# Kernel optimization log

Hardware: AMD Instinct MI355X
Metric: run time of the kernel (lower is better)

## Reference

```python
import jax, jax.numpy as jnp
import numpy as np

N, K, F_IN, F_OUT, P = 50000, 32, 64, 64, 3


def setup_inputs() -> dict:
    key = jax.random.key(0)
    k1, k2, k3, k4, k5 = jax.random.split(key, 5)
    h = jax.random.normal(k1, (N, F_IN), dtype=jnp.float32)
    pos = jax.random.normal(k2, (N, P), dtype=jnp.float32)
    neighbor_idx = jax.random.randint(k3, (N, K), 0, N, dtype=jnp.int32)
    weight = jax.random.normal(k4, (K * F_IN, F_OUT), dtype=jnp.float32) * 0.02
    bias_p = jax.random.normal(k5, (1, F_OUT), dtype=jnp.float32) * 0.02
    return {"h": h, "pos": pos, "neighbor_idx": neighbor_idx,
            "weight": weight, "bias_p": bias_p}


def reference(h, pos, neighbor_idx, weight, bias_p):
    n, k = neighbor_idx.shape
    msgs = h[neighbor_idx]                      # [N, K, F_IN] gather
    diff = pos[:, None, :] - pos[neighbor_idx]  # [N, K, P]
    sq = jnp.sum(diff * diff, axis=2, keepdims=True)  # [N, K, 1]
    # torch: dist[dist==0] = 0.5 ; safe-sqrt avoids NaN grads at 0
    dist = jnp.where(sq == 0.0, 0.5, jnp.sqrt(jnp.where(sq == 0.0, 1.0, sq)))
    wow = (msgs / dist).reshape(n, k * h.shape[1])  # [N, K*F_IN]
    h1 = wow @ weight + bias_p                   # [N, F_OUT]
    return jax.nn.leaky_relu(h1, negative_slope=0.01)
```

## Files before the change

### kernel.cpp

```cpp
#include <hip/hip_runtime.h>


#define N_NODES 50000
#define KN      32
#define FIN     64
#define FOUT    64
#define MTILE   64

typedef __attribute__((ext_vector_type(4))) float    f32x4;
typedef __attribute__((ext_vector_type(8))) _Float16 f16x8;

static __device__ __forceinline__ f16x8 dec8i(unsigned int x, unsigned int y) {
    union { unsigned int w[4]; f16x8 v; } r;
    unsigned int xh = x >> 16, yh = y >> 16;
    r.w[0] = 0x64006400u | ((x  & 0xFFu) << 2) | ((x  & 0xFF00u) << 10);
    r.w[1] = 0x64006400u | ((xh & 0xFFu) << 2) | ((xh & 0xFF00u) << 10);
    r.w[2] = 0x64006400u | ((y  & 0xFFu) << 2) | ((y  & 0xFF00u) << 10);
    r.w[3] = 0x64006400u | ((yh & 0xFFu) << 2) | ((yh & 0xFF00u) << 10);
    return r.v;
}

__global__ void k_prep(const float* __restrict__ w, _Float16* __restrict__ wf,
                       const float* __restrict__ h, unsigned char* __restrict__ hq,
                       const float* __restrict__ pos, float4* __restrict__ posx) {
    __shared__ float s_w[64 * 64];
    const int tid = threadIdx.x;
    if (blockIdx.x < 32) {
        const int kn = blockIdx.x;
        for (int p = tid; p < 64 * 64; p += 256)
            s_w[p] = w[kn * 64 * 64 + p];
        __syncthreads();
        const int t = tid >> 6, lane = tid & 63;
        const int lm = lane & 15, q = lane >> 4;
        #pragma unroll
        for (int jh = 0; jh < 2; ++jh) {
            f16x8 o;
            #pragma unroll
            for (int i = 0; i < 8; ++i)
                o[i] = (_Float16)s_w[(q * 16 + jh * 8 + i) * 64 + t * 16 + lm];
            *(f16x8*)(wf + ((kn * 2 + jh) * 4 + t) * 512 + lane * 8) = o;
        }
    } else {
        const int r   = (blockIdx.x - 32) * 64 + (tid >> 2);
        const int sub = tid & 3;
        if (r < N_NODES) {
            const float* hr = h + (size_t)r * FIN + sub * 16;
            float v[16];
            float amax = 0.f;
            #pragma unroll
            for (int i = 0; i < 4; ++i) {
                float4 t4 = ((const float4*)hr)[i];
                v[i * 4 + 0] = t4.x; v[i * 4 + 1] = t4.y;
                v[i * 4 + 2] = t4.z; v[i * 4 + 3] = t4.w;
                amax = fmaxf(amax, fmaxf(fmaxf(fabsf(t4.x), fabsf(t4.y)),
                                         fmaxf(fabsf(t4.z), fabsf(t4.w))));
            }
            amax = fmaxf(amax, __shfl_xor(amax, 1));
            amax = fmaxf(amax, __shfl_xor(amax, 2));
            float scale = fmaxf(amax, 1e-30f) * (1.0f / 126.0f);
            float inv   = 126.0f / fmaxf(amax, 1e-30f);
            union { unsigned char c[16]; uint4 u4; } o;
            #pragma unroll
            for (int i = 0; i < 16; ++i) {
                int q8 = __float2int_rn(v[i] * inv);
                o.c[i] = (unsigned char)(q8 + 128);
            }
            *(uint4*)(hq + (size_t)r * 64 + sub * 16) = o.u4;
            if (sub == 0) {
                float4 px;
                px.x = pos[r * 3 + 0]; px.y = pos[r * 3 + 1]; px.z = pos[r * 3 + 2];
                px.w = scale;
                posx[r] = px;
            }
        }
    }
}

__global__ __launch_bounds__(256, 3) void k_main(
        const unsigned char* __restrict__ hq,
        const float4*        __restrict__ posx,
        const int*           __restrict__ nidx,
        const _Float16*      __restrict__ wf,
        const float*         __restrict__ bias,
        float*               __restrict__ out)
{
    __shared__ __align__(16) char smem[2 * 64 * 68 * 4];
    int2*  s_e   = (int2*)smem;
    float* s_red = (float*)smem;

    const int tid = threadIdx.x;
    const int m0  = blockIdx.x * MTILE;

    for (int p = tid; p < MTILE * KN; p += 256) {
        int m = p & 63, k = p >> 6;
        int node = m0 + m;
        int idx = 0; float c1 = 0.f;
        if (node < N_NODES) {
            idx = nidx[node * KN + k];
            float4 pn = posx[node];
            float4 pi = posx[idx];
            float dx = pn.x - pi.x, dy = pn.y - pi.y, dz = pn.z - pi.z;
            float sq = dx * dx + dy * dy + dz * dz;
            float scl = (sq == 0.f) ? 2.0f : rsqrtf(sq);
            c1 = pi.w * scl * 0.25f;
        }
        s_e[k * MTILE + m] = make_int2(idx, __float_as_int(c1));
    }
    __syncthreads();

    const int lane = tid & 63, kg = tid >> 6;
    const int lm = lane & 15, q = lane >> 4;

    const _Float16* pb = wf + lane * 8;

    f32x4 acc[4][4] = {};

    const int kn0 = kg * 8;
    int2 e0 = s_e[kn0 * MTILE + lm];
    int2 e1 = s_e[kn0 * MTILE + 16 + lm];
    int2 e2 = s_e[kn0 * MTILE + 32 + lm];
    int2 e3 = s_e[kn0 * MTILE + 48 + lm];
    uint4 d0 = *(const uint4*)(hq + (size_t)e0.x * 64 + q * 16);
    uint4 d1 = *(const uint4*)(hq + (size_t)e1.x * 64 + q * 16);
    uint4 d2 = *(const uint4*)(hq + (size_t)e2.x * 64 + q * 16);
    uint4 d3 = *(const uint4*)(hq + (size_t)e3.x * 64 + q * 16);

    #pragma unroll 1
    for (int j = 0; j < 8; ++j) {
        const int kn = kg * 8 + j;

        int2 ne0, ne1, ne2, ne3;
        uint4 nd0, nd1, nd2, nd3;
        if (j < 7) {
            const int knn = kn + 1;
            ne0 = s_e[knn * MTILE + lm];
            ne1 = s_e[knn * MTILE + 16 + lm];
            ne2 = s_e[knn * MTILE + 32 + lm];
            ne3 = s_e[knn * MTILE + 48 + lm];
            nd0 = *(const uint4*)(hq + (size_t)ne0.x * 64 + q * 16);
            nd1 = *(const uint4*)(hq + (size_t)ne1.x * 64 + q * 16);
            nd2 = *(const uint4*)(hq + (size_t)ne2.x * 64 + q * 16);
            nd3 = *(const uint4*)(hq + (size_t)ne3.x * 64 + q * 16);
        }

        const _Float16 c0 = (_Float16)__int_as_float(e0.y);
        const _Float16 c1 = (_Float16)__int_as_float(e1.y);
        const _Float16 c2 = (_Float16)__int_as_float(e2.y);
        const _Float16 c3 = (_Float16)__int_as_float(e3.y);
        const _Float16 K = (_Float16)1536.0f;

        {
            const _Float16* pbb = pb + (kn * 2 + 0) * 2048;
            f16x8 b0 = *(const f16x8*)(pbb);
            f16x8 b1 = *(const f16x8*)(pbb + 512);
            f16x8 b2 = *(const f16x8*)(pbb + 1024);
            f16x8 b3 = *(const f16x8*)(pbb + 1536);
            f16x8 a0 = (dec8i(d0.x, d0.y) - K) * c0;
            f16x8 a1 = (dec8i(d1.x, d1.y) - K) * c1;
            f16x8 a2 = (dec8i(d2.x, d2.y) - K) * c2;
            f16x8 a3 = (dec8i(d3.x, d3.y) - K) * c3;
            acc[0][0] = __builtin_amdgcn_mfma_f32_16x16x32_f16(a0, b0, acc[0][0], 0, 0, 0);
            acc[0][1] = __builtin_amdgcn_mfma_f32_16x16x32_f16(a0, b1, acc[0][1], 0, 0, 0);
            acc[0][2] = __builtin_amdgcn_mfma_f32_16x16x32_f16(a0, b2, acc[0][2], 0, 0, 0);
            acc[0][3] = __builtin_amdgcn_mfma_f32_16x16x32_f16(a0, b3, acc[0][3], 0, 0, 0);
            acc[1][0] = __builtin_amdgcn_mfma_f32_16x16x32_f16(a1, b0, acc[1][0], 0, 0, 0);
            acc[1][1] = __builtin_amdgcn_mfma_f32_16x16x32_f16(a1, b1, acc[1][1], 0, 0, 0);
            acc[1][2] = __builtin_amdgcn_mfma_f32_16x16x32_f16(a1, b2, acc[1][2], 0, 0, 0);
            acc[1][3] = __builtin_amdgcn_mfma_f32_16x16x32_f16(a1, b3, acc[1][3], 0, 0, 0);
            acc[2][0] = __builtin_amdgcn_mfma_f32_16x16x32_f16(a2, b0, acc[2][0], 0, 0, 0);
            acc[2][1] = __builtin_amdgcn_mfma_f32_16x16x32_f16(a2, b1, acc[2][1], 0, 0, 0);
            acc[2][2] = __builtin_amdgcn_mfma_f32_16x16x32_f16(a2, b2, acc[2][2], 0, 0, 0);
            acc[2][3] = __builtin_amdgcn_mfma_f32_16x16x32_f16(a2, b3, acc[2][3], 0, 0, 0);
            acc[3][0] = __builtin_amdgcn_mfma_f32_16x16x32_f16(a3, b0, acc[3][0], 0, 0, 0);
            acc[3][1] = __builtin_amdgcn_mfma_f32_16x16x32_f16(a3, b1, acc[3][1], 0, 0, 0);
            acc[3][2] = __builtin_amdgcn_mfma_f32_16x16x32_f16(a3, b2, acc[3][2], 0, 0, 0);
            acc[3][3] = __builtin_amdgcn_mfma_f32_16x16x32_f16(a3, b3, acc[3][3], 0, 0, 0);
        }
        {
            const _Float16* pbb = pb + (kn * 2 + 1) * 2048;
            f16x8 b0 = *(const f16x8*)(pbb);
            f16x8 b1 = *(const f16x8*)(pbb + 512);
            f16x8 b2 = *(const f16x8*)(pbb + 1024);
            f16x8 b3 = *(const f16x8*)(pbb + 1536);
            f16x8 a0 = (dec8i(d0.z, d0.w) - K) * c0;
            f16x8 a1 = (dec8i(d1.z, d1.w) - K) * c1;
            f16x8 a2 = (dec8i(d2.z, d2.w) - K) * c2;
            f16x8 a3 = (dec8i(d3.z, d3.w) - K) * c3;
            acc[0][0] = __builtin_amdgcn_mfma_f32_16x16x32_f16(a0, b0, acc[0][0], 0, 0, 0);
            acc[0][1] = __builtin_amdgcn_mfma_f32_16x16x32_f16(a0, b1, acc[0][1], 0, 0, 0);
            acc[0][2] = __builtin_amdgcn_mfma_f32_16x16x32_f16(a0, b2, acc[0][2], 0, 0, 0);
            acc[0][3] = __builtin_amdgcn_mfma_f32_16x16x32_f16(a0, b3, acc[0][3], 0, 0, 0);
            acc[1][0] = __builtin_amdgcn_mfma_f32_16x16x32_f16(a1, b0, acc[1][0], 0, 0, 0);
            acc[1][1] = __builtin_amdgcn_mfma_f32_16x16x32_f16(a1, b1, acc[1][1], 0, 0, 0);
            acc[1][2] = __builtin_amdgcn_mfma_f32_16x16x32_f16(a1, b2, acc[1][2], 0, 0, 0);
            acc[1][3] = __builtin_amdgcn_mfma_f32_16x16x32_f16(a1, b3, acc[1][3], 0, 0, 0);
            acc[2][0] = __builtin_amdgcn_mfma_f32_16x16x32_f16(a2, b0, acc[2][0], 0, 0, 0);
            acc[2][1] = __builtin_amdgcn_mfma_f32_16x16x32_f16(a2, b1, acc[2][1], 0, 0, 0);
            acc[2][2] = __builtin_amdgcn_mfma_f32_16x16x32_f16(a2, b2, acc[2][2], 0, 0, 0);
            acc[2][3] = __builtin_amdgcn_mfma_f32_16x16x32_f16(a2, b3, acc[2][3], 0, 0, 0);
            acc[3][0] = __builtin_amdgcn_mfma_f32_16x16x32_f16(a3, b0, acc[3][0], 0, 0, 0);
            acc[3][1] = __builtin_amdgcn_mfma_f32_16x16x32_f16(a3, b1, acc[3][1], 0, 0, 0);
            acc[3][2] = __builtin_amdgcn_mfma_f32_16x16x32_f16(a3, b2, acc[3][2], 0, 0, 0);
            acc[3][3] = __builtin_amdgcn_mfma_f32_16x16x32_f16(a3, b3, acc[3][3], 0, 0, 0);
        }

        if (j < 7) {
            e0 = ne0; e1 = ne1; e2 = ne2; e3 = ne3;
            d0 = nd0; d1 = nd1; d2 = nd2; d3 = nd3;
        }
    }

    __syncthreads();

    float* reg = s_red + (kg & 1) * (64 * 68);
    if (kg < 2) {
        #pragma unroll
        for (int mt = 0; mt < 4; ++mt)
            #pragma unroll
            for (int t = 0; t < 4; ++t)
                #pragma unroll
                for (int r = 0; r < 4; ++r)
                    reg[(mt * 16 + q * 4 + r) * 68 + t * 16 + lm] = acc[mt][t][r];
    }
    __syncthreads();
    if (kg >= 2) {
        #pragma unroll
        for (int mt = 0; mt < 4; ++mt)
            #pragma unroll
            for (int t = 0; t < 4; ++t)
                #pragma unroll
                for (int r = 0; r < 4; ++r)
                    reg[(mt * 16 + q * 4 + r) * 68 + t * 16 + lm] += acc[mt][t][r];
    }
    __syncthreads();

    const int row = tid >> 2, c0e = (tid & 3) * 16;
    const int node = m0 + row;
    if (node < N_NODES) {
        #pragma unroll
        for (int i = 0; i < 4; ++i) {
            int c = c0e + i * 4;
            f32x4 v0 = *(const f32x4*)(s_red + row * 68 + c);
            f32x4 v1 = *(const f32x4*)(s_red + 64 * 68 + row * 68 + c);
            f32x4 bb = *(const f32x4*)(bias + c);
            f32x4 o = v0 + v1 + bb;
            #pragma unroll
            for (int jj = 0; jj < 4; ++jj) o[jj] = o[jj] > 0.f ? o[jj] : 0.01f * o[jj];
            *(f32x4*)(out + node * FOUT + c) = o;
        }
    }
}

extern "C" void kernel_launch(void* const* d_in, const int* in_sizes, int n_in,
                              void* d_out, int out_size, void* d_ws, size_t ws_size,
                              hipStream_t stream) {
    const float* h    = (const float*)d_in[0];
    const float* pos  = (const float*)d_in[1];
    const int*   nidx = (const int*)d_in[2];
    const float* w    = (const float*)d_in[3];
    const float* bias = (const float*)d_in[4];
    float* out = (float*)d_out;

    _Float16*      wf   = (_Float16*)d_ws;
    unsigned char* hq   = (unsigned char*)d_ws + 262144;
    float4*        posx = (float4*)((char*)d_ws + 262144 + 3200000);

    const int h_blocks = (N_NODES + 63) / 64;
    k_prep<<<32 + h_blocks, 256, 0, stream>>>(w, wf, h, hq, pos, posx);
    k_main<<<(N_NODES + MTILE - 1) / MTILE, 256, 0, stream>>>(hq, posx, nidx, wf, bias, out);
}
```

Before: 121.3 us.

## Make edge prep wave-local, drop gather prefetch, raise occupancy to 4 blocks

Each wave now computes the edge entries (neighbor index and scale) only for its own 8-neighbor slice, using a padded row-major shared layout with pitch 35. This removes the block-wide barrier between edge prep and the MFMA loop. The register double-buffering of the next iteration's gathers is removed and launch bounds go from 3 to 4 blocks per SM. Gather latency is now meant to be hidden by more resident waves instead of software prefetch. The risk is exposed latency on each gather plus possible register spills under the tighter register budget.

```diff
diff --git a/kernel.cpp b/kernel.cpp
--- a/kernel.cpp
+++ b/kernel.cpp
@@ -6,6 +6,7 @@
 #define FIN     64
 #define FOUT    64
 #define MTILE   64
+#define EPITCH  35
 
 typedef __attribute__((ext_vector_type(4))) float    f32x4;
 typedef __attribute__((ext_vector_type(8))) _Float16 f16x8;
@@ -76,7 +77,7 @@
     }
 }
 
-__global__ __launch_bounds__(256, 3) void k_main(
+__global__ __launch_bounds__(256, 4) void k_main(
         const unsigned char* __restrict__ hq,
         const float4*        __restrict__ posx,
         const int*           __restrict__ nidx,
@@ -90,13 +91,17 @@
 
     const int tid = threadIdx.x;
     const int m0  = blockIdx.x * MTILE;
-
-    for (int p = tid; p < MTILE * KN; p += 256) {
-        int m = p & 63, k = p >> 6;
+    const int lane = tid & 63, kg = tid >> 6;
+    const int lm = lane & 15, q = lane >> 4;
+
+    for (int it = 0; it < 8; ++it) {
+        int pp = it * 64 + lane;
+        int m  = pp >> 3;
+        int kn = kg * 8 + (pp & 7);
         int node = m0 + m;
         int idx = 0; float c1 = 0.f;
         if (node < N_NODES) {
-            idx = nidx[node * KN + k];
+            idx = nidx[node * KN + kn];
             float4 pn = posx[node];
             float4 pi = posx[idx];
             float dx = pn.x - pi.x, dy = pn.y - pi.y, dz = pn.z - pi.z;
@@ -104,45 +109,24 @@
             float scl = (sq == 0.f) ? 2.0f : rsqrtf(sq);
             c1 = pi.w * scl * 0.25f;
         }
-        s_e[k * MTILE + m] = make_int2(idx, __float_as_int(c1));
-    }
-    __syncthreads();
-
-    const int lane = tid & 63, kg = tid >> 6;
-    const int lm = lane & 15, q = lane >> 4;
+        s_e[m * EPITCH + kn] = make_int2(idx, __float_as_int(c1));
+    }
 
     const _Float16* pb = wf + lane * 8;
 
     f32x4 acc[4][4] = {};
-
-    const int kn0 = kg * 8;
-    int2 e0 = s_e[kn0 * MTILE + lm];
-    int2 e1 = s_e[kn0 * MTILE + 16 + lm];
-    int2 e2 = s_e[kn0 * MTILE + 32 + lm];
-    int2 e3 = s_e[kn0 * MTILE + 48 + lm];
-    uint4 d0 = *(const uint4*)(hq + (size_t)e0.x * 64 + q * 16);
-    uint4 d1 = *(const uint4*)(hq + (size_t)e1.x * 64 + q * 16);
-    uint4 d2 = *(const uint4*)(hq + (size_t)e2.x * 64 + q * 16);
-    uint4 d3 = *(const uint4*)(hq + (size_t)e3.x * 64 + q * 16);
 
     #pragma unroll 1
     for (int j = 0; j < 8; ++j) {
         const int kn = kg * 8 + j;
-
-        int2 ne0, ne1, ne2, ne3;
-        uint4 nd0, nd1, nd2, nd3;
-        if (j < 7) {
-            const int knn = kn + 1;
-            ne0 = s_e[knn * MTILE + lm];
-            ne1 = s_e[knn * MTILE + 16 + lm];
-            ne2 = s_e[knn * MTILE + 32 + lm];
-            ne3 = s_e[knn * MTILE + 48 + lm];
-            nd0 = *(const uint4*)(hq + (size_t)ne0.x * 64 + q * 16);
-            nd1 = *(const uint4*)(hq + (size_t)ne1.x * 64 + q * 16);
-            nd2 = *(const uint4*)(hq + (size_t)ne2.x * 64 + q * 16);
-            nd3 = *(const uint4*)(hq + (size_t)ne3.x * 64 + q * 16);
-        }
-
+        int2 e0 = s_e[(lm     ) * EPITCH + kn];
+        int2 e1 = s_e[(lm + 16) * EPITCH + kn];
+        int2 e2 = s_e[(lm + 32) * EPITCH + kn];
+        int2 e3 = s_e[(lm + 48) * EPITCH + kn];
+        uint4 d0 = *(const uint4*)(hq + (size_t)e0.x * 64 + q * 16);
+        uint4 d1 = *(const uint4*)(hq + (size_t)e1.x * 64 + q * 16);
+        uint4 d2 = *(const uint4*)(hq + (size_t)e2.x * 64 + q * 16);
+        uint4 d3 = *(const uint4*)(hq + (size_t)e3.x * 64 + q * 16);
         const _Float16 c0 = (_Float16)__int_as_float(e0.y);
         const _Float16 c1 = (_Float16)__int_as_float(e1.y);
         const _Float16 c2 = (_Float16)__int_as_float(e2.y);
@@ -203,11 +187,6 @@
             acc[3][2] = __builtin_amdgcn_mfma_f32_16x16x32_f16(a3, b2, acc[3][2], 0, 0, 0);
             acc[3][3] = __builtin_amdgcn_mfma_f32_16x16x32_f16(a3, b3, acc[3][3], 0, 0, 0);
         }
-
-        if (j < 7) {
-            e0 = ne0; e1 = ne1; e2 = ne2; e3 = ne3;
-            d0 = nd0; d1 = nd1; d2 = nd2; d3 = nd3;
-        }
     }
 
     __syncthreads();
```

New measurement: 114.3 us (median of 2 runs). 1.06x faster.
